# Kernel tuning notes

Hardware: AMD Instinct MI355X
Metric: run time of the kernel (lower is better)

Reference implementation:

```python
import jax, jax.numpy as jnp
import numpy as np

# config
D_MODEL, D_A, D_B, R, N, D, S, D_K = 512, 256, 256, 8, 2048, 4608, 4, 64
HID = 2 * D_MODEL
U_END = D_B * R
V_END = U_END + R * D_A
B_END = V_END + D_B
LAMBDA_SHARP = 1.0
TEMPERATURE = 1.0
LN_EPS = 1e-6


def _lecun(key, shape):
    fan_in = shape[-2] if len(shape) > 1 else shape[0]
    return jax.random.normal(key, shape, dtype=jnp.float32) * (1.0 / np.sqrt(fan_in))


def setup_inputs() -> dict:
    key = jax.random.key(0)
    ks = jax.random.split(key, 12)
    return {
        'x': jax.random.normal(ks[0], (256, D_MODEL), dtype=jnp.float32),
        'pool_vectors': 0.01 * jax.random.normal(ks[1], (N, D), dtype=jnp.float32),
        'A_w0': _lecun(ks[2], (D_MODEL, HID)), 'A_b0': jnp.zeros(HID),
        'A_w1': _lecun(ks[3], (HID, D_A)), 'A_b1': jnp.zeros(D_A),
        'W_Q': _lecun(ks[4], (S, D_A, D_K)),
        'W_K': _lecun(ks[5], (S, D, D_K)),
        'aspect_logits': jnp.zeros(S),
        'tau': jnp.asarray(0.5, dtype=jnp.float32),
        'W_base': 0.01 * jax.random.normal(ks[6], (D_B, D_A), dtype=jnp.float32),
        'b_base': jnp.zeros(D_B),
        'gamma': jnp.asarray(0.1, dtype=jnp.float32),
        'ln_scale': jnp.ones(D_A), 'ln_bias': jnp.zeros(D_A),
        'B_w0': _lecun(ks[7], (D_A, HID)), 'B_b0': jnp.zeros(HID),
        'B_w1': _lecun(ks[8], (HID, D_MODEL)), 'B_b1': jnp.zeros(D_MODEL),
    }


def _forward(x, pool_vectors, A_w0, A_b0, A_w1, A_b1, W_Q, W_K, aspect_logits, tau,
             W_base, b_base, gamma, ln_scale, ln_bias, B_w0, B_b0, B_w1, B_b1):
    # Part A MLP
    h_A = jax.nn.gelu(x @ A_w0 + A_b0) @ A_w1 + A_b1                     # [b, d_A]
    # Multi-aspect retrieval
    queries = jnp.einsum('bd,adq->baq', h_A, W_Q)                        # [b, S, d_k]
    keys = jnp.einsum('np,apq->naq', pool_vectors, W_K)                  # [N, S, d_k]
    q_norm = queries / (jnp.linalg.norm(queries, axis=-1, keepdims=True) + 1e-8)
    k_norm = keys / (jnp.linalg.norm(keys, axis=-1, keepdims=True) + 1e-8)
    sims = jnp.einsum('baq,naq->bna', q_norm, k_norm)                    # [b, N, S]
    w = jax.nn.softmax(aspect_logits)
    scores = jnp.einsum('bna,a->bn', sims, w)                            # [b, N]
    g = jax.nn.sigmoid(LAMBDA_SHARP * (scores - tau))
    alpha_raw = g * jnp.exp(scores / TEMPERATURE)
    alpha = alpha_raw / (jnp.sum(alpha_raw, axis=-1, keepdims=True) + 1e-8)
    # Assemble per-sample weight matrix from low-rank factors
    U = pool_vectors[:, :U_END].reshape(N, D_B, R)
    V = pool_vectors[:, U_END:V_END].reshape(N, R, D_A)
    bias = pool_vectors[:, V_END:B_END]                                  # [N, d_B]
    UV = jnp.einsum('ndr,nre->nde', U, V)                                # [N, d_B, d_A]
    W_assembled = W_base[None] + jnp.einsum('bn,nde->bde', alpha, UV)    # [b, d_B, d_A]
    b_assembled = b_base[None] + jnp.einsum('bn,nd->bd', alpha, bias)
    # Middle layer: dynamic matmul + residual + LayerNorm
    h_t = jnp.einsum('ba,bca->bc', h_A, W_assembled) + b_assembled
    y = h_A + gamma * h_t
    mu = jnp.mean(y, axis=-1, keepdims=True)
    var = jnp.mean((y - mu) ** 2, axis=-1, keepdims=True)
    h_mid = (y - mu) / jnp.sqrt(var + LN_EPS) * ln_scale + ln_bias
    # Part B MLP
    output = jax.nn.gelu(h_mid @ B_w0 + B_b0) @ B_w1 + B_b1
    return output, alpha, W_assembled, keys


def reference(x, pool_vectors, A_w0, A_b0, A_w1, A_b1, W_Q, W_K, aspect_logits, tau,
              W_base, b_base, gamma, ln_scale, ln_bias, B_w0, B_b0, B_w1, B_b1):
    return _forward(x, pool_vectors, A_w0, A_b0, A_w1, A_b1, W_Q, W_K, aspect_logits, tau,
                    W_base, b_base, gamma, ln_scale, ln_bias, B_w0, B_b0, B_w1, B_b1)
```

## Files before the change

kernel.cpp:

```cpp
#include <hip/hip_runtime.h>
#include <hip/hip_bf16.h>
#include <math.h>

#define N_POOL 2048
#define D_POOL 4608

typedef __hip_bfloat16 bf16;
typedef __attribute__((ext_vector_type(8))) short bf16x8;
typedef __attribute__((ext_vector_type(4))) float f32x4;
typedef __attribute__((ext_vector_type(4))) unsigned short u16x4;

#define IX 0
#define IPOOL 1
#define IAW0 2
#define IAB0 3
#define IAW1 4
#define IAB1 5
#define IWQ 6
#define IWK 7
#define ILOG 8
#define ITAU 9
#define IWBASE 10
#define IBBASE 11
#define IGAMMA 12
#define ILNS 13
#define ILNB 14
#define IBW0 15
#define IBB0 16
#define IBW1 17
#define IBB1 18

__device__ inline float wsum(float v) {
#pragma unroll
    for (int off = 32; off > 0; off >>= 1) v += __shfl_xor(v, off, 64);
    return v;
}
__device__ inline float ldin(const void* p, size_t i, int f) {
    if (f) return __bfloat162float(((const bf16*)p)[i]);
    return ((const float*)p)[i];
}
__device__ inline float gelu_f(float x) {
    float t = tanhf(0.7978845608028654f * (x + 0.044715f * x * x * x));
    return 0.5f * x * (1.0f + t);
}
__device__ inline unsigned short bfbits(float f) {
    __hip_bfloat16 h = __float2bfloat16(f);
    return *reinterpret_cast<unsigned short*>(&h);
}

struct P19 { const void* p[19]; long n[19]; };

__global__ void detect_all(P19 ip, int* flags) {
    const int j = blockIdx.x;
    const unsigned short* u = (const unsigned short*)ip.p[j];
    long nelem = ip.n[j];
    long nhalf = nelem >> 1; if (nhalf < 1) nhalf = 1;
    long kstep = (nhalf + 8191) >> 13; if (kstep < 1) kstep = 1;
    int W = 0, S = 0, Z = 0, O = 0, C = 0;
    for (long k = threadIdx.x; k * kstep < nhalf; k += 256) {
        long i = k * kstep * 2;
        unsigned short ev = u[i], od = u[i + 1];
        int e = (ev >> 7) & 0xFF;
        if (ev == 0) Z++;
        else if (e >= 90 && e <= 141) S++;
        else W++;
        if (od) O++;
        C++;
    }
    __shared__ int sw[256], ss[256], sz[256], so[256], sc[256];
    sw[threadIdx.x] = W; ss[threadIdx.x] = S; sz[threadIdx.x] = Z;
    so[threadIdx.x] = O; sc[threadIdx.x] = C;
    __syncthreads();
    if (threadIdx.x == 0) {
        int tw = 0, ts = 0, tz = 0, to = 0, tc = 0;
        for (int i = 0; i < 256; i++) {
            tw += sw[i]; ts += ss[i]; tz += sz[i]; to += so[i]; tc += sc[i];
        }
        int f;
        if (tw * 16 > tc) f = 0;
        else if (ts == 0 && tw == 0) f = (to > 0) ? 0 : 1;
        else f = (ts >= tz) ? 1 : 0;
        flags[j] = f;
    }
}

template <int TRANSB>
__global__ __launch_bounds__(256) void gemm64(
    const void* __restrict__ A, int lda, int afi,
    const void* __restrict__ B, int ldb, int bfi, size_t boffs,
    const void* __restrict__ bias, int bifi,
    float* __restrict__ C, int ldc,
    int M, int N, int K, int act, const int* __restrict__ flags)
{
    const int fa = (afi >= 0) ? flags[afi] : 0;
    const int fb = (bfi >= 0) ? flags[bfi] : 0;
    const int fbias = (bifi >= 0) ? flags[bifi] : 0;
    __shared__ __align__(16) float As[16][68];
    __shared__ __align__(16) float Bs[16][68];
    const int tid = threadIdx.x;
    const int tx = tid & 15, ty = tid >> 4;
    const int bx = blockIdx.x, by = blockIdx.y;
    float acc[4][4] = {};
    for (int k0 = 0; k0 < K; k0 += 16) {
#pragma unroll
        for (int i = 0; i < 4; i++) {
            int idx = tid + i * 256;
            int m = idx >> 4, kk = idx & 15;
            As[kk][m] = ldin(A, (size_t)(by * 64 + m) * lda + k0 + kk, fa);
        }
#pragma unroll
        for (int i = 0; i < 4; i++) {
            int idx = tid + i * 256;
            if (TRANSB) {
                int nn2 = idx >> 4, kk = idx & 15;
                Bs[kk][nn2] = ldin(B, boffs + (size_t)(bx * 64 + nn2) * ldb + k0 + kk, fb);
            } else {
                int kk = idx >> 6, nn2 = idx & 63;
                Bs[kk][nn2] = ldin(B, boffs + (size_t)(k0 + kk) * ldb + bx * 64 + nn2, fb);
            }
        }
        __syncthreads();
#pragma unroll
        for (int kk = 0; kk < 16; kk++) {
            float4 av4 = *(const float4*)&As[kk][ty * 4];
            float4 bv4 = *(const float4*)&Bs[kk][tx * 4];
            float av[4] = {av4.x, av4.y, av4.z, av4.w};
            float bv[4] = {bv4.x, bv4.y, bv4.z, bv4.w};
#pragma unroll
            for (int i = 0; i < 4; i++)
#pragma unroll
                for (int j = 0; j < 4; j++) acc[i][j] += av[i] * bv[j];
        }
        __syncthreads();
    }
#pragma unroll
    for (int i = 0; i < 4; i++) {
        int m = by * 64 + ty * 4 + i;
#pragma unroll
        for (int j = 0; j < 4; j++) {
            int n = bx * 64 + tx * 4 + j;
            float v = acc[i][j];
            if (bias) v += ldin(bias, n, fbias);
            if (act == 1) v = gelu_f(v);
            C[(size_t)m * ldc + n] = v;
        }
    }
}

template <int TRANSB>
__global__ __launch_bounds__(256) void gemm64_splitk(
    const void* __restrict__ A, int lda, int afi,
    const void* __restrict__ B, int ldb, int bfi, size_t boffs,
    float* __restrict__ C, int ldc, int KC, const int* __restrict__ flags)
{
    const int fa = (afi >= 0) ? flags[afi] : 0;
    const int fb = (bfi >= 0) ? flags[bfi] : 0;
    __shared__ __align__(16) float As[16][68];
    __shared__ __align__(16) float Bs[16][68];
    const int tid = threadIdx.x;
    const int tx = tid & 15, ty = tid >> 4;
    const int bx = blockIdx.x, by = blockIdx.y;
    const int kbeg = blockIdx.z * KC;
    float acc[4][4] = {};
    for (int k0 = kbeg; k0 < kbeg + KC; k0 += 16) {
#pragma unroll
        for (int i = 0; i < 4; i++) {
            int idx = tid + i * 256;
            int m = idx >> 4, kk = idx & 15;
            As[kk][m] = ldin(A, (size_t)(by * 64 + m) * lda + k0 + kk, fa);
        }
#pragma unroll
        for (int i = 0; i < 4; i++) {
            int idx = tid + i * 256;
            if (TRANSB) {
                int nn2 = idx >> 4, kk = idx & 15;
                Bs[kk][nn2] = ldin(B, boffs + (size_t)(bx * 64 + nn2) * ldb + k0 + kk, fb);
            } else {
                int kk = idx >> 6, nn2 = idx & 63;
                Bs[kk][nn2] = ldin(B, boffs + (size_t)(k0 + kk) * ldb + bx * 64 + nn2, fb);
            }
        }
        __syncthreads();
#pragma unroll
        for (int kk = 0; kk < 16; kk++) {
            float4 av4 = *(const float4*)&As[kk][ty * 4];
            float4 bv4 = *(const float4*)&Bs[kk][tx * 4];
            float av[4] = {av4.x, av4.y, av4.z, av4.w};
            float bv[4] = {bv4.x, bv4.y, bv4.z, bv4.w};
#pragma unroll
            for (int i = 0; i < 4; i++)
#pragma unroll
                for (int j = 0; j < 4; j++) acc[i][j] += av[i] * bv[j];
        }
        __syncthreads();
    }
#pragma unroll
    for (int i = 0; i < 4; i++) {
        int m = by * 64 + ty * 4 + i;
#pragma unroll
        for (int j = 0; j < 4; j++) {
            int n = bx * 64 + tx * 4 + j;
            atomicAdd(&C[(size_t)m * ldc + n], acc[i][j]);
        }
    }
}

__global__ __launch_bounds__(256) void gemm_mfma_atomic(
    const unsigned short* __restrict__ A, int lda,
    const unsigned short* __restrict__ Bmat, int ldb,
    float* __restrict__ C, int ldc, int KC)
{
    const int m0 = blockIdx.x * 128;
    const int n0 = blockIdx.y * 64;
    const unsigned short* B = Bmat + (size_t)blockIdx.y * 64 * ldb;
    const int kbeg = blockIdx.z * KC;
    const int t = threadIdx.x, w = t >> 6, l = t & 63;
    const int q = l >> 4, l16 = l & 15;
    f32x4 acc[2][4] = {};
    for (int k0 = kbeg; k0 < kbeg + KC; k0 += 32) {
        bf16x8 afr[2], bfr[4];
#pragma unroll
        for (int mt = 0; mt < 2; mt++)
            afr[mt] = *(const bf16x8*)&A[(size_t)(m0 + w * 32 + mt * 16 + l16) * lda + k0 + q * 8];
#pragma unroll
        for (int nt = 0; nt < 4; nt++)
            bfr[nt] = *(const bf16x8*)&B[(size_t)(nt * 16 + l16) * ldb + k0 + q * 8];
#pragma unroll
        for (int mt = 0; mt < 2; mt++)
#pragma unroll
            for (int nt = 0; nt < 4; nt++)
                acc[mt][nt] = __builtin_amdgcn_mfma_f32_16x16x32_bf16(
                    afr[mt], bfr[nt], acc[mt][nt], 0, 0, 0);
    }
#pragma unroll
    for (int mt = 0; mt < 2; mt++)
#pragma unroll
        for (int nt = 0; nt < 4; nt++)
#pragma unroll
            for (int r = 0; r < 4; r++) {
                int m = m0 + w * 32 + mt * 16 + q * 4 + r;
                atomicAdd(&C[(size_t)m * ldc + n0 + nt * 16 + l16], acc[mt][nt][r]);
            }
}

__global__ __launch_bounds__(256) void pool2bf(
    const void* __restrict__ pool, const int* __restrict__ flags,
    unsigned short* __restrict__ pb)
{
    const int fp = flags[IPOOL];
    const size_t total = (size_t)N_POOL * D_POOL;
    for (size_t i = ((size_t)blockIdx.x * 256 + threadIdx.x) * 4; i < total;
         i += (size_t)gridDim.x * 1024) {
        u16x4 o;
        if (fp == 0) {
            float4 v = *(const float4*)((const float*)pool + i);
            o[0] = bfbits(v.x); o[1] = bfbits(v.y); o[2] = bfbits(v.z); o[3] = bfbits(v.w);
        } else {
            o = *(const u16x4*)((const unsigned short*)pool + i);
        }
        *(u16x4*)&pb[i] = o;
    }
}

__global__ __launch_bounds__(256) void wk2bfT(
    const void* __restrict__ W_K, const int* __restrict__ flags,
    unsigned short* __restrict__ out)
{
    const int fk = flags[IWK];
    const int a = blockIdx.y, kb = blockIdx.x, t = threadIdx.x;
#pragma unroll
    for (int i = 0; i < 16; i++) {
        int idx = i * 256 + t;
        int kk = idx >> 6, qq = idx & 63;
        float v = ldin(W_K, (size_t)a * 294912 + (size_t)(kb * 64 + kk) * 64 + qq, fk);
        out[(size_t)(a * 64 + qq) * 4608 + kb * 64 + kk] = bfbits(v);
    }
}

__global__ __launch_bounds__(256) void bias2bfT(
    const void* __restrict__ pool, const int* __restrict__ flags,
    unsigned short* __restrict__ out)
{
    const int fp = flags[IPOOL];
    const int nb = blockIdx.x, cb = blockIdx.y, t = threadIdx.x;
#pragma unroll
    for (int i = 0; i < 16; i++) {
        int idx = i * 256 + t;
        int nn = idx >> 6, cc = idx & 63;
        float v = ldin(pool, (size_t)(nb * 64 + nn) * 4608 + 4096 + cb * 64 + cc, fp);
        out[(size_t)(cb * 64 + cc) * 2048 + nb * 64 + nn] = bfbits(v);
    }
}

__global__ __launch_bounds__(256) void init_bias_kernel(
    float* __restrict__ C, const void* __restrict__ bias, int bifi,
    const int* __restrict__ flags, int N, int total)
{
    int i = blockIdx.x * 256 + threadIdx.x;
    if (i >= total) return;
    float v = 0.f;
    if (bias) v = ldin(bias, i % N, (bifi >= 0) ? flags[bifi] : 0);
    C[i] = v;
}

__global__ __launch_bounds__(256) void gelu_kernel(float* __restrict__ buf, int total)
{
    int i = blockIdx.x * 256 + threadIdx.x;
    if (i < total) buf[i] = gelu_f(buf[i]);
}

__global__ __launch_bounds__(256) void knorm_kernel(
    const float* __restrict__ keys, float* __restrict__ kn)
{
    const int n = blockIdx.x;
    const int a = threadIdx.x >> 6, q = threadIdx.x & 63;
    float v = keys[(size_t)n * 256 + a * 64 + q];
    float ss = wsum(v * v);
    kn[(size_t)n * 256 + a * 64 + q] = v / (sqrtf(ss) + 1e-8f);
}

__global__ void softmax4_kernel(const void* __restrict__ logits,
                                const int* __restrict__ flags, float* __restrict__ w) {
    if (threadIdx.x == 0) {
        int f = flags[ILOG];
        float l0 = ldin(logits, 0, f), l1 = ldin(logits, 1, f);
        float l2 = ldin(logits, 2, f), l3 = ldin(logits, 3, f);
        float m = fmaxf(fmaxf(l0, l1), fmaxf(l2, l3));
        float e0 = expf(l0 - m), e1 = expf(l1 - m), e2 = expf(l2 - m), e3 = expf(l3 - m);
        float s = e0 + e1 + e2 + e3;
        w[0] = e0 / s; w[1] = e1 / s; w[2] = e2 / s; w[3] = e3 / s;
    }
}

__global__ __launch_bounds__(256) void queries_kernel(
    const float* __restrict__ hA, const void* __restrict__ W_Q,
    const int* __restrict__ flags, const float* __restrict__ w, float* __restrict__ qw)
{
    const int f = flags[IWQ];
    const int b = blockIdx.x;
    const int a = threadIdx.x >> 6, q = threadIdx.x & 63;
    const float* ha = hA + b * 256;
    float s = 0.f;
#pragma unroll 4
    for (int d = 0; d < 256; d++)
        s += ha[d] * ldin(W_Q, (size_t)a * 16384 + (size_t)d * 64 + q, f);
    float nrm = sqrtf(wsum(s * s));
    qw[b * 256 + a * 64 + q] = s / (nrm + 1e-8f) * w[a];
}

__global__ __launch_bounds__(256) void alpha_kernel(
    const float* __restrict__ scores, const void* __restrict__ tau_p,
    const int* __restrict__ flags,
    float* __restrict__ alpha_out, unsigned short* __restrict__ alphaT,
    unsigned short* __restrict__ alphaB)
{
    const int b = blockIdx.x;
    const int tid = threadIdx.x;
    const float tauv = ldin(tau_p, 0, flags[ITAU]);
    float ar[8];
    float lsum = 0.f;
#pragma unroll
    for (int i = 0; i < 8; i++) {
        int n = i * 256 + tid;
        float s = scores[b * 2048 + n];
        float g = 1.f / (1.f + expf(-(s - tauv)));
        ar[i] = g * expf(s);
        lsum += ar[i];
    }
    __shared__ float sb[4];
    float wsv = wsum(lsum);
    if ((tid & 63) == 0) sb[tid >> 6] = wsv;
    __syncthreads();
    float tot = sb[0] + sb[1] + sb[2] + sb[3];
    float inv = 1.f / (tot + 1e-8f);
#pragma unroll
    for (int i = 0; i < 8; i++) {
        int n = i * 256 + tid;
        float al = ar[i] * inv;
        alpha_out[b * 2048 + n] = al;
        unsigned short bb = bfbits(al);
        alphaT[(size_t)(n >> 3) * 2048 + b * 8 + (n & 7)] = bb;
        alphaB[(size_t)b * 2048 + n] = bb;
    }
}

#define QW 520
__global__ __launch_bounds__(256, 2) void assemble_mfma(
    const unsigned short* __restrict__ alphaT,
    const void* __restrict__ pool,
    const void* __restrict__ W_base,
    const int* __restrict__ flags,
    float* __restrict__ Wout)
{
    const int fp = flags[IPOOL], fw = flags[IWBASE];
    const int lid = blockIdx.x;
    const int xcd = lid & 7, idx = lid >> 3;
    const int dt = idx & 31;
    const int et = ((idx >> 5) << 3) + xcd;
    const int d0 = dt * 8, e0 = et * 16;
    const int t = threadIdx.x;
    const int w = t >> 6, l = t & 63;
    const int q = l >> 4, l16 = l & 15;

    const int nl  = t >> 3;
    const int sub = t & 7;
    const int dlp = sub >> 1;
    const int eh  = sub & 1;
    const int jj  = nl & 7;

    __shared__ __align__(16) float Us[2][32][76];
    __shared__ __align__(16) float Vs[2][32][132];
    __shared__ __align__(16) unsigned short uvb[8][QW];

    const float4* pool4 = (const float4*)pool;

    f32x4 acc[4][8] = {};

    auto load_stage = [&](int n0, float4* st) {
#pragma unroll
        for (int i = 0; i < 2; i++) {
            int f = i * 256 + t;
            int n = n0 + (f >> 4);
            int q4 = f & 15;
            if (fp == 0) {
                st[i] = pool4[(size_t)n * 1152 + d0 * 2 + q4];
            } else {
                size_t base = (size_t)n * 4608 + (size_t)d0 * 8 + q4 * 4;
                st[i] = make_float4(ldin(pool, base, 1), ldin(pool, base + 1, 1),
                                    ldin(pool, base + 2, 1), ldin(pool, base + 3, 1));
            }
        }
#pragma unroll
        for (int i = 0; i < 4; i++) {
            int f = i * 256 + t;
            int n = n0 + (f >> 5);
            int r = (f & 31) >> 2, e4 = f & 3;
            if (fp == 0) {
                st[2 + i] = pool4[(size_t)n * 1152 + 512 + r * 64 + (e0 >> 2) + e4];
            } else {
                size_t base = (size_t)n * 4608 + 2048 + (size_t)r * 256 + e0 + e4 * 4;
                st[2 + i] = make_float4(ldin(pool, base, 1), ldin(pool, base + 1, 1),
                                        ldin(pool, base + 2, 1), ldin(pool, base + 3, 1));
            }
        }
    };
    auto store_stage = [&](int bp, const float4* st) {
#pragma unroll
        for (int i = 0; i < 2; i++) {
            int f = i * 256 + t;
            *(float4*)&Us[bp][f >> 4][(f & 15) * 4] = st[i];
        }
#pragma unroll
        for (int i = 0; i < 4; i++) {
            int f = i * 256 + t;
            int r = (f & 31) >> 2, e4 = f & 3;
            *(float4*)&Vs[bp][f >> 5][r * 16 + e4 * 4] = st[2 + i];
        }
    };

    {
        float4 st[6];
        load_stage(0, st);
        store_stage(0, st);
    }
    __syncthreads();

    int p = 0;
    for (int step = 0; step < 64; step++) {
        const int n0 = step * 32;
        float4 stn[6];
        if (step < 63) load_stage(n0 + 32, stn);

        bf16x8 afr[4];
#pragma unroll
        for (int mt = 0; mt < 4; mt++) {
            const unsigned short* ap =
                alphaT + (size_t)(step * 4 + q) * 2048 + (w * 64 + mt * 16 + l16) * 8;
            afr[mt] = *(const bf16x8*)ap;
        }

        {
            const float* Ur = &Us[p][nl][dlp * 16];
            float4 Ua = *(const float4*)(Ur);
            float4 Ub = *(const float4*)(Ur + 4);
            float4 Uc = *(const float4*)(Ur + 8);
            float4 Ud = *(const float4*)(Ur + 12);
            float U0[8] = {Ua.x, Ua.y, Ua.z, Ua.w, Ub.x, Ub.y, Ub.z, Ub.w};
            float U1[8] = {Uc.x, Uc.y, Uc.z, Uc.w, Ud.x, Ud.y, Ud.z, Ud.w};
            float uv0[8] = {0.f, 0.f, 0.f, 0.f, 0.f, 0.f, 0.f, 0.f};
            float uv1[8] = {0.f, 0.f, 0.f, 0.f, 0.f, 0.f, 0.f, 0.f};
#pragma unroll
            for (int r = 0; r < 8; r++) {
                float4 va = *(const float4*)&Vs[p][nl][r * 16 + eh * 8];
                float4 vb = *(const float4*)&Vs[p][nl][r * 16 + eh * 8 + 4];
                uv0[0] += U0[r] * va.x; uv0[1] += U0[r] * va.y;
                uv0[2] += U0[r] * va.z; uv0[3] += U0[r] * va.w;
                uv0[4] += U0[r] * vb.x; uv0[5] += U0[r] * vb.y;
                uv0[6] += U0[r] * vb.z; uv0[7] += U0[r] * vb.w;
                uv1[0] += U1[r] * va.x; uv1[1] += U1[r] * va.y;
                uv1[2] += U1[r] * va.z; uv1[3] += U1[r] * va.w;
                uv1[4] += U1[r] * vb.x; uv1[5] += U1[r] * vb.y;
                uv1[6] += U1[r] * vb.z; uv1[7] += U1[r] * vb.w;
            }
            const int cg0 = dlp * 2, cg1 = cg0 + 1;
            const int wbase = w * 128 + eh * 64 + jj;
#pragma unroll
            for (int i = 0; i < 8; i++) {
                uvb[cg0][wbase + i * 8] = bfbits(uv0[i]);
                uvb[cg1][wbase + i * 8] = bfbits(uv1[i]);
            }
        }
        __syncthreads();

        bf16x8 bfr[8];
#pragma unroll
        for (int cg = 0; cg < 8; cg++)
            bfr[cg] = *(const bf16x8*)&uvb[cg][l * 8];
        if (step < 63) store_stage(p ^ 1, stn);
#pragma unroll
        for (int mt = 0; mt < 4; mt++)
#pragma unroll
            for (int cg = 0; cg < 8; cg++)
                acc[mt][cg] = __builtin_amdgcn_mfma_f32_16x16x32_bf16(
                    afr[mt], bfr[cg], acc[mt][cg], 0, 0, 0);
        __syncthreads();
        p ^= 1;
    }

    float wb[8];
#pragma unroll
    for (int cg = 0; cg < 8; cg++)
        wb[cg] = ldin(W_base, (size_t)(d0 + cg) * 256 + e0 + l16, fw);
#pragma unroll
    for (int mt = 0; mt < 4; mt++) {
#pragma unroll
        for (int cg = 0; cg < 8; cg++) {
            size_t col = (size_t)(d0 + cg) * 256 + e0 + l16;
#pragma unroll
            for (int r = 0; r < 4; r++) {
                int b = w * 64 + mt * 16 + q * 4 + r;
                Wout[(size_t)b * 65536 + col] = acc[mt][cg][r] + wb[cg];
            }
        }
    }
}

__global__ __launch_bounds__(256) void hty_kernel(
    const float* __restrict__ Wout, const float* __restrict__ hA,
    const float* __restrict__ bass, const void* __restrict__ gamma_p,
    const int* __restrict__ flags, float* __restrict__ y)
{
    const int b = blockIdx.y;
    const int c = blockIdx.x * 4 + (threadIdx.x >> 6);
    const int lane = threadIdx.x & 63;
    const float4 wv = ((const float4*)(Wout + ((size_t)b * 65536 + c * 256)))[lane];
    const float4 h4 = ((const float4*)(hA + b * 256))[lane];
    float s = wv.x * h4.x + wv.y * h4.y + wv.z * h4.z + wv.w * h4.w;
    s = wsum(s);
    if (lane == 0) {
        float ht = s + bass[b * 256 + c];
        y[b * 256 + c] = hA[b * 256 + c] + ldin(gamma_p, 0, flags[IGAMMA]) * ht;
    }
}

__global__ __launch_bounds__(256) void ln_kernel(
    const float* __restrict__ y, const void* __restrict__ ln_scale,
    const void* __restrict__ ln_bias, const int* __restrict__ flags,
    float* __restrict__ hmid)
{
    const int fs = flags[ILNS], fb = flags[ILNB];
    const int b = blockIdx.x, tid = threadIdx.x;
    float v = y[b * 256 + tid];
    __shared__ float s1b[4], s2b[4];
    float w1 = wsum(v), w2 = wsum(v * v);
    if ((tid & 63) == 0) { s1b[tid >> 6] = w1; s2b[tid >> 6] = w2; }
    __syncthreads();
    float mu = (s1b[0] + s1b[1] + s1b[2] + s1b[3]) * (1.f / 256.f);
    float ex2 = (s2b[0] + s2b[1] + s2b[2] + s2b[3]) * (1.f / 256.f);
    float var = ex2 - mu * mu;
    float inv = 1.f / sqrtf(var + 1e-6f);
    hmid[b * 256 + tid] = (v - mu) * inv * ldin(ln_scale, tid, fs)
                        + ldin(ln_bias, tid, fb);
}

extern "C" void kernel_launch(void* const* d_in, const int* in_sizes, int n_in,
                              void* d_out, int out_size, void* d_ws, size_t ws_size,
                              hipStream_t stream)
{
    (void)out_size; (void)n_in;
    const void* x      = d_in[0];
    const void* pool   = d_in[1];
    const void* A_w0   = d_in[2];
    const void* A_b0   = d_in[3];
    const void* A_w1   = d_in[4];
    const void* A_b1   = d_in[5];
    const void* W_Q    = d_in[6];
    const void* W_K    = d_in[7];
    const void* logits = d_in[8];
    const void* tau    = d_in[9];
    const void* W_base = d_in[10];
    const void* b_base = d_in[11];
    const void* gamma  = d_in[12];
    const void* ln_s   = d_in[13];
    const void* ln_b   = d_in[14];
    const void* B_w0   = d_in[15];
    const void* B_b0   = d_in[16];
    const void* B_w1   = d_in[17];
    const void* B_b1   = d_in[18];

    float* out       = (float*)d_out;
    float* out0      = out;
    float* out_alpha = out + 131072;
    float* out_W     = out + 655360;
    float* out_keys  = out + 17432576;

    float* ws = (float*)d_ws;
    int*   flagp   = (int*)d_ws;
    float* ws_w    = ws + 32;
    float* ws_hA   = ws + 64;
    float* ws_qw   = ws + 65600;
    float* ws_bass = ws + 131136;
    float* ws_y    = ws + 196672;
    float* ws_hmid = ws + 262208;
    unsigned short* alpha_bf = (unsigned short*)(ws + 327744);

    size_t wsf = ws_size / 4;
    bool full = wsf >= 1638464;
    float* slotA;
    float* slotB;
    float* T1;
    float* scr = (float*)out_W;
    if (full) {
        slotA = ws + 589888;
        slotB = ws + 1114176;
        T1    = slotA;
    } else {
        slotA = scr;
        slotB = scr + 524288;
        T1    = (float*)alpha_bf;
    }
    float* G      = slotA;
    float* scores = slotA;
    float* kn     = slotB;

    unsigned short* poolbf = (unsigned short*)(scr + 2097152);
    unsigned short* wkbT   = (unsigned short*)(scr + 7340032);
    unsigned short* biasT  = (unsigned short*)(scr + 8388608);
    unsigned short* alphaB = (unsigned short*)(scr + 8912896);

    P19 ip;
    for (int i = 0; i < 19; i++) { ip.p[i] = d_in[i]; ip.n[i] = in_sizes[i]; }
    detect_all<<<19, 256, 0, stream>>>(ip, flagp);
    softmax4_kernel<<<1, 64, 0, stream>>>(logits, flagp, ws_w);
    pool2bf<<<2048, 256, 0, stream>>>(pool, flagp, poolbf);
    wk2bfT<<<dim3(72, 4), 256, 0, stream>>>(W_K, flagp, wkbT);
    bias2bfT<<<dim3(32, 4), 256, 0, stream>>>(pool, flagp, biasT);
    init_bias_kernel<<<1024, 256, 0, stream>>>(G, A_b0, IAB0, flagp, 1024, 262144);
    gemm64_splitk<0><<<dim3(16, 4, 4), 256, 0, stream>>>(
        x, 512, IX, A_w0, 1024, IAW0, 0,
        G, 1024, 128, flagp);
    gelu_kernel<<<1024, 256, 0, stream>>>(G, 262144);
    init_bias_kernel<<<256, 256, 0, stream>>>(ws_hA, A_b1, IAB1, flagp, 256, 65536);
    gemm64_splitk<0><<<dim3(4, 4, 8), 256, 0, stream>>>(
        G, 1024, -1, A_w1, 256, IAW1, 0,
        ws_hA, 256, 128, flagp);
    init_bias_kernel<<<2048, 256, 0, stream>>>(out_keys, nullptr, -1, flagp, 256, 524288);
    gemm_mfma_atomic<<<dim3(16, 4, 16), 256, 0, stream>>>(
        poolbf, 4608, wkbT, 4608, out_keys, 256, 288);
    knorm_kernel<<<2048, 256, 0, stream>>>(out_keys, kn);
    queries_kernel<<<256, 256, 0, stream>>>(ws_hA, W_Q, flagp, ws_w, ws_qw);
    gemm64<1><<<dim3(32, 4), 256, 0, stream>>>(
        ws_qw, 256, -1, kn, 256, -1, 0, nullptr, -1,
        scores, 2048, 256, 2048, 256, 0, flagp);
    alpha_kernel<<<256, 256, 0, stream>>>(scores, tau, flagp, out_alpha, alpha_bf, alphaB);
    init_bias_kernel<<<256, 256, 0, stream>>>(ws_bass, b_base, IBBASE, flagp, 256, 65536);
    gemm_mfma_atomic<<<dim3(2, 4, 8), 256, 0, stream>>>(
        alphaB, 2048, biasT, 2048, ws_bass, 256, 256);
    assemble_mfma<<<512, 256, 0, stream>>>(alpha_bf, pool, W_base, flagp, out_W);
    hty_kernel<<<dim3(64, 256), 256, 0, stream>>>(out_W, ws_hA, ws_bass, gamma, flagp, ws_y);
    ln_kernel<<<256, 256, 0, stream>>>(ws_y, ln_s, ln_b, flagp, ws_hmid);
    init_bias_kernel<<<1024, 256, 0, stream>>>(T1, B_b0, IBB0, flagp, 1024, 262144);
    gemm64_splitk<0><<<dim3(16, 4, 2), 256, 0, stream>>>(
        ws_hmid, 256, -1, B_w0, 1024, IBW0, 0,
        T1, 1024, 128, flagp);
    gelu_kernel<<<1024, 256, 0, stream>>>(T1, 262144);
    init_bias_kernel<<<512, 256, 0, stream>>>(out0, B_b1, IBB1, flagp, 512, 131072);
    gemm64_splitk<0><<<dim3(8, 4, 4), 256, 0, stream>>>(
        T1, 1024, -1, B_w1, 512, IBW1, 0,
        out0, 512, 256, flagp);
}
```

Baseline: 626.1 us.

## Move Part A MLP, queries and scores GEMMs to bf16 MFMA with fused epilogues

```diff
diff --git a/kernel.cpp b/kernel.cpp
--- a/kernel.cpp
+++ b/kernel.cpp
@@ -85,69 +85,6 @@
 }
 
 template <int TRANSB>
-__global__ __launch_bounds__(256) void gemm64(
-    const void* __restrict__ A, int lda, int afi,
-    const void* __restrict__ B, int ldb, int bfi, size_t boffs,
-    const void* __restrict__ bias, int bifi,
-    float* __restrict__ C, int ldc,
-    int M, int N, int K, int act, const int* __restrict__ flags)
-{
-    const int fa = (afi >= 0) ? flags[afi] : 0;
-    const int fb = (bfi >= 0) ? flags[bfi] : 0;
-    const int fbias = (bifi >= 0) ? flags[bifi] : 0;
-    __shared__ __align__(16) float As[16][68];
-    __shared__ __align__(16) float Bs[16][68];
-    const int tid = threadIdx.x;
-    const int tx = tid & 15, ty = tid >> 4;
-    const int bx = blockIdx.x, by = blockIdx.y;
-    float acc[4][4] = {};
-    for (int k0 = 0; k0 < K; k0 += 16) {
-#pragma unroll
-        for (int i = 0; i < 4; i++) {
-            int idx = tid + i * 256;
-            int m = idx >> 4, kk = idx & 15;
-            As[kk][m] = ldin(A, (size_t)(by * 64 + m) * lda + k0 + kk, fa);
-        }
-#pragma unroll
-        for (int i = 0; i < 4; i++) {
-            int idx = tid + i * 256;
-            if (TRANSB) {
-                int nn2 = idx >> 4, kk = idx & 15;
-                Bs[kk][nn2] = ldin(B, boffs + (size_t)(bx * 64 + nn2) * ldb + k0 + kk, fb);
-            } else {
-                int kk = idx >> 6, nn2 = idx & 63;
-                Bs[kk][nn2] = ldin(B, boffs + (size_t)(k0 + kk) * ldb + bx * 64 + nn2, fb);
-            }
-        }
-        __syncthreads();
-#pragma unroll
-        for (int kk = 0; kk < 16; kk++) {
-            float4 av4 = *(const float4*)&As[kk][ty * 4];
-            float4 bv4 = *(const float4*)&Bs[kk][tx * 4];
-            float av[4] = {av4.x, av4.y, av4.z, av4.w};
-            float bv[4] = {bv4.x, bv4.y, bv4.z, bv4.w};
-#pragma unroll
-            for (int i = 0; i < 4; i++)
-#pragma unroll
-                for (int j = 0; j < 4; j++) acc[i][j] += av[i] * bv[j];
-        }
-        __syncthreads();
-    }
-#pragma unroll
-    for (int i = 0; i < 4; i++) {
-        int m = by * 64 + ty * 4 + i;
-#pragma unroll
-        for (int j = 0; j < 4; j++) {
-            int n = bx * 64 + tx * 4 + j;
-            float v = acc[i][j];
-            if (bias) v += ldin(bias, n, fbias);
-            if (act == 1) v = gelu_f(v);
-            C[(size_t)m * ldc + n] = v;
-        }
-    }
-}
-
-template <int TRANSB>
 __global__ __launch_bounds__(256) void gemm64_splitk(
     const void* __restrict__ A, int lda, int afi,
     const void* __restrict__ B, int ldb, int bfi, size_t boffs,
@@ -243,6 +180,54 @@
             }
 }
 
+template <int ACT>
+__global__ __launch_bounds__(256) void gemm_mfma_fused(
+    const unsigned short* __restrict__ A, int lda,
+    const unsigned short* __restrict__ Bmat, int ldb,
+    const void* __restrict__ bias, int bifi, const int* __restrict__ flags,
+    float* __restrict__ Cf, unsigned short* __restrict__ Cbf,
+    int ldc, int K)
+{
+    const int m0 = blockIdx.x * 128;
+    const int n0 = blockIdx.y * 64;
+    const unsigned short* B = Bmat + (size_t)blockIdx.y * 64 * ldb;
+    const int t = threadIdx.x, w = t >> 6, l = t & 63;
+    const int q = l >> 4, l16 = l & 15;
+    f32x4 acc[2][4] = {};
+    for (int k0 = 0; k0 < K; k0 += 32) {
+        bf16x8 afr[2], bfr[4];
+#pragma unroll
+        for (int mt = 0; mt < 2; mt++)
+            afr[mt] = *(const bf16x8*)&A[(size_t)(m0 + w * 32 + mt * 16 + l16) * lda + k0 + q * 8];
+#pragma unroll
+        for (int nt = 0; nt < 4; nt++)
+            bfr[nt] = *(const bf16x8*)&B[(size_t)(nt * 16 + l16) * ldb + k0 + q * 8];
+#pragma unroll
+        for (int mt = 0; mt < 2; mt++)
+#pragma unroll
+            for (int nt = 0; nt < 4; nt++)
+                acc[mt][nt] = __builtin_amdgcn_mfma_f32_16x16x32_bf16(
+                    afr[mt], bfr[nt], acc[mt][nt], 0, 0, 0);
+    }
+    float bv[4];
+#pragma unroll
+    for (int nt = 0; nt < 4; nt++)
+        bv[nt] = bias ? ldin(bias, n0 + nt * 16 + l16, (bifi >= 0) ? flags[bifi] : 0) : 0.f;
+#pragma unroll
+    for (int mt = 0; mt < 2; mt++)
+#pragma unroll
+        for (int nt = 0; nt < 4; nt++)
+#pragma unroll
+            for (int r = 0; r < 4; r++) {
+                int m = m0 + w * 32 + mt * 16 + q * 4 + r;
+                int n = n0 + nt * 16 + l16;
+                float v = acc[mt][nt][r] + bv[nt];
+                if (ACT == 1) v = gelu_f(v);
+                if (Cf)  Cf[(size_t)m * ldc + n] = v;
+                if (Cbf) Cbf[(size_t)m * ldc + n] = bfbits(v);
+            }
+}
+
 __global__ __launch_bounds__(256) void pool2bf(
     const void* __restrict__ pool, const int* __restrict__ flags,
     unsigned short* __restrict__ pb)
@@ -262,6 +247,46 @@
     }
 }
 
+__global__ __launch_bounds__(256) void cvt2bf(
+    const void* __restrict__ src, int fi, const int* __restrict__ flags,
+    unsigned short* __restrict__ dst, int total)
+{
+    const int f = (fi >= 0) ? flags[fi] : 0;
+    int i = (blockIdx.x * 256 + threadIdx.x) * 4;
+    if (i >= total) return;
+    if (f == 0) {
+        float4 v = *(const float4*)((const float*)src + i);
+        u16x4 o;
+        o[0] = bfbits(v.x); o[1] = bfbits(v.y); o[2] = bfbits(v.z); o[3] = bfbits(v.w);
+        *(u16x4*)&dst[i] = o;
+    } else {
+        *(u16x4*)&dst[i] = *(const u16x4*)((const unsigned short*)src + i);
+    }
+}
+
+__global__ __launch_bounds__(256) void transp_bf(
+    const void* __restrict__ src, int fi, const int* __restrict__ flags,
+    unsigned short* __restrict__ dst, int rows, int cols)
+{
+    const int f = (fi >= 0) ? flags[fi] : 0;
+    const size_t zoff = (size_t)blockIdx.z * rows * cols;
+    const int rb = blockIdx.y * 64, cb = blockIdx.x * 64;
+    __shared__ float tile[64][65];
+    const int t = threadIdx.x;
+    const int lr = t >> 6, lc = t & 63;
+#pragma unroll
+    for (int i = 0; i < 16; i++) {
+        int r = i * 4 + lr;
+        tile[r][lc] = ldin(src, zoff + (size_t)(rb + r) * cols + cb + lc, f);
+    }
+    __syncthreads();
+#pragma unroll
+    for (int i = 0; i < 16; i++) {
+        int c = i * 4 + lr;
+        dst[zoff + (size_t)(cb + c) * rows + rb + lc] = bfbits(tile[lc][c]);
+    }
+}
+
 __global__ __launch_bounds__(256) void wk2bfT(
     const void* __restrict__ W_K, const int* __restrict__ flags,
     unsigned short* __restrict__ out)
@@ -310,13 +335,24 @@
 }
 
 __global__ __launch_bounds__(256) void knorm_kernel(
-    const float* __restrict__ keys, float* __restrict__ kn)
+    const float* __restrict__ keys, unsigned short* __restrict__ knbf)
 {
     const int n = blockIdx.x;
     const int a = threadIdx.x >> 6, q = threadIdx.x & 63;
     float v = keys[(size_t)n * 256 + a * 64 + q];
     float ss = wsum(v * v);
-    kn[(size_t)n * 256 + a * 64 + q] = v / (sqrtf(ss) + 1e-8f);
+    knbf[(size_t)n * 256 + a * 64 + q] = bfbits(v / (sqrtf(ss) + 1e-8f));
+}
+
+__global__ __launch_bounds__(256) void qnorm_kernel(
+    const float* __restrict__ qraw, const float* __restrict__ w,
+    unsigned short* __restrict__ qwbf)
+{
+    const int b = blockIdx.x;
+    const int a = threadIdx.x >> 6, q = threadIdx.x & 63;
+    float v = qraw[b * 256 + a * 64 + q];
+    float ss = wsum(v * v);
+    qwbf[b * 256 + a * 64 + q] = bfbits(v / (sqrtf(ss) + 1e-8f) * w[a]);
 }
 
 __global__ void softmax4_kernel(const void* __restrict__ logits,
@@ -330,22 +366,6 @@
         float s = e0 + e1 + e2 + e3;
         w[0] = e0 / s; w[1] = e1 / s; w[2] = e2 / s; w[3] = e3 / s;
     }
-}
-
-__global__ __launch_bounds__(256) void queries_kernel(
-    const float* __restrict__ hA, const void* __restrict__ W_Q,
-    const int* __restrict__ flags, const float* __restrict__ w, float* __restrict__ qw)
-{
-    const int f = flags[IWQ];
-    const int b = blockIdx.x;
-    const int a = threadIdx.x >> 6, q = threadIdx.x & 63;
-    const float* ha = hA + b * 256;
-    float s = 0.f;
-#pragma unroll 4
-    for (int d = 0; d < 256; d++)
-        s += ha[d] * ldin(W_Q, (size_t)a * 16384 + (size_t)d * 64 + q, f);
-    float nrm = sqrtf(wsum(s * s));
-    qw[b * 256 + a * 64 + q] = s / (nrm + 1e-8f) * w[a];
 }
 
 __global__ __launch_bounds__(256) void alpha_kernel(
@@ -639,10 +659,17 @@
         slotB = scr + 524288;
         T1    = (float*)alpha_bf;
     }
-    float* G      = slotA;
     float* scores = slotA;
-    float* kn     = slotB;
-
+    unsigned short* knbf = (unsigned short*)slotB;
+
+    unsigned short* xbf    = (unsigned short*)(scr + 1048576);
+    unsigned short* aw0T   = (unsigned short*)(scr + 1114112);
+    unsigned short* aw1T   = (unsigned short*)(scr + 1376256);
+    unsigned short* wqT    = (unsigned short*)(scr + 1507328);
+    unsigned short* Gbf    = (unsigned short*)(scr + 1540096);
+    unsigned short* hAbf   = (unsigned short*)(scr + 1671168);
+    float*          qraw   = scr + 1703936;
+    unsigned short* qwbf   = (unsigned short*)(scr + 1769472);
     unsigned short* poolbf = (unsigned short*)(scr + 2097152);
     unsigned short* wkbT   = (unsigned short*)(scr + 7340032);
     unsigned short* biasT  = (unsigned short*)(scr + 8388608);
@@ -655,23 +682,23 @@
     pool2bf<<<2048, 256, 0, stream>>>(pool, flagp, poolbf);
     wk2bfT<<<dim3(72, 4), 256, 0, stream>>>(W_K, flagp, wkbT);
     bias2bfT<<<dim3(32, 4), 256, 0, stream>>>(pool, flagp, biasT);
-    init_bias_kernel<<<1024, 256, 0, stream>>>(G, A_b0, IAB0, flagp, 1024, 262144);
-    gemm64_splitk<0><<<dim3(16, 4, 4), 256, 0, stream>>>(
-        x, 512, IX, A_w0, 1024, IAW0, 0,
-        G, 1024, 128, flagp);
-    gelu_kernel<<<1024, 256, 0, stream>>>(G, 262144);
-    init_bias_kernel<<<256, 256, 0, stream>>>(ws_hA, A_b1, IAB1, flagp, 256, 65536);
-    gemm64_splitk<0><<<dim3(4, 4, 8), 256, 0, stream>>>(
-        G, 1024, -1, A_w1, 256, IAW1, 0,
-        ws_hA, 256, 128, flagp);
+    cvt2bf<<<128, 256, 0, stream>>>(x, IX, flagp, xbf, 131072);
+    transp_bf<<<dim3(16, 8, 1), 256, 0, stream>>>(A_w0, IAW0, flagp, aw0T, 512, 1024);
+    transp_bf<<<dim3(4, 16, 1), 256, 0, stream>>>(A_w1, IAW1, flagp, aw1T, 1024, 256);
+    transp_bf<<<dim3(1, 4, 4), 256, 0, stream>>>(W_Q, IWQ, flagp, wqT, 256, 64);
+    gemm_mfma_fused<1><<<dim3(2, 16), 256, 0, stream>>>(
+        xbf, 512, aw0T, 512, A_b0, IAB0, flagp, nullptr, Gbf, 1024, 512);
+    gemm_mfma_fused<0><<<dim3(2, 4), 256, 0, stream>>>(
+        Gbf, 1024, aw1T, 1024, A_b1, IAB1, flagp, ws_hA, hAbf, 256, 1024);
     init_bias_kernel<<<2048, 256, 0, stream>>>(out_keys, nullptr, -1, flagp, 256, 524288);
     gemm_mfma_atomic<<<dim3(16, 4, 16), 256, 0, stream>>>(
         poolbf, 4608, wkbT, 4608, out_keys, 256, 288);
-    knorm_kernel<<<2048, 256, 0, stream>>>(out_keys, kn);
-    queries_kernel<<<256, 256, 0, stream>>>(ws_hA, W_Q, flagp, ws_w, ws_qw);
-    gemm64<1><<<dim3(32, 4), 256, 0, stream>>>(
-        ws_qw, 256, -1, kn, 256, -1, 0, nullptr, -1,
-        scores, 2048, 256, 2048, 256, 0, flagp);
+    knorm_kernel<<<2048, 256, 0, stream>>>(out_keys, knbf);
+    gemm_mfma_fused<0><<<dim3(2, 4), 256, 0, stream>>>(
+        hAbf, 256, wqT, 256, nullptr, -1, flagp, qraw, nullptr, 256, 256);
+    qnorm_kernel<<<256, 256, 0, stream>>>(qraw, ws_w, qwbf);
+    gemm_mfma_fused<0><<<dim3(2, 32), 256, 0, stream>>>(
+        qwbf, 256, knbf, 256, nullptr, -1, flagp, scores, nullptr, 2048, 256);
     alpha_kernel<<<256, 256, 0, stream>>>(scores, tau, flagp, out_alpha, alpha_bf, alphaB);
     init_bias_kernel<<<256, 256, 0, stream>>>(ws_bass, b_base, IBBASE, flagp, 256, 65536);
     gemm_mfma_atomic<<<dim3(2, 4, 8), 256, 0, stream>>>(
```

After: 567.7 us. 1.1x faster.
